# Optimization experiments

Measured on AMD Instinct MI355X. Metric: run time of the kernel, lower is better.

The kernel has to match this reference:

```python
import jax, jax.numpy as jnp
import numpy as np

N_NODES = 50000
N_EDGES = 800000
IN_FEATS = 128
SAGE_HID = 512
H_FEATS = 128
MLP_HID = 32
N_PARTS = 8


def setup_inputs() -> dict:
    key = jax.random.key(0)
    ks = jax.random.split(key, 16)
    s = 0.05
    return {
        "features": jax.random.normal(ks[0], (N_NODES, IN_FEATS), jnp.float32),
        "src": jax.random.randint(ks[1], (N_EDGES,), 0, N_NODES),
        "dst": jax.random.randint(ks[2], (N_EDGES,), 0, N_NODES),
        # SAGEConv layer 1 (in_feats -> 512): fc_self has bias, fc_neigh no bias
        "W1_self": jax.random.normal(ks[3], (IN_FEATS, SAGE_HID), jnp.float32) * s,
        "W1_neigh": jax.random.normal(ks[4], (IN_FEATS, SAGE_HID), jnp.float32) * s,
        "b1": jnp.zeros((SAGE_HID,), jnp.float32),
        # SAGEConv layer 2 (512 -> h_feats)
        "W2_self": jax.random.normal(ks[5], (SAGE_HID, H_FEATS), jnp.float32) * s,
        "W2_neigh": jax.random.normal(ks[6], (SAGE_HID, H_FEATS), jnp.float32) * s,
        "b2": jnp.zeros((H_FEATS,), jnp.float32),
        # Partitioning MLP
        "Wp1": jax.random.normal(ks[7], (H_FEATS, MLP_HID), jnp.float32) * s,
        "bp1": jnp.zeros((MLP_HID,), jnp.float32),
        "Wp2": jax.random.normal(ks[8], (MLP_HID, N_PARTS), jnp.float32) * s,
        "bp2": jnp.zeros((N_PARTS,), jnp.float32),
    }


def _sage_mean(x, src, dst, deg_inv, W_self, W_neigh, b):
    # gather source-node features per edge, sum by destination, divide by in-degree
    agg = jax.ops.segment_sum(jnp.take(x, src, axis=0), dst, num_segments=N_NODES)
    agg = agg * deg_inv[:, None]
    return x @ W_self + agg @ W_neigh + b


def reference(features, src, dst, W1_self, W1_neigh, b1, W2_self, W2_neigh, b2,
              Wp1, bp1, Wp2, bp2):
    deg = jax.ops.segment_sum(jnp.ones_like(dst, dtype=features.dtype), dst,
                              num_segments=N_NODES)
    deg_inv = 1.0 / jnp.maximum(deg, 1.0)
    h = jax.nn.relu(_sage_mean(features, src, dst, deg_inv, W1_self, W1_neigh, b1))
    h = jax.nn.relu(_sage_mean(h, src, dst, deg_inv, W2_self, W2_neigh, b2))
    x = jax.nn.relu(h @ Wp1 + bp1)
    logits = x @ Wp2 + bp2
    return jax.nn.softmax(logits, axis=1)
```

## Files before the change

### kernel.cpp

```cpp
#include <hip/hip_runtime.h>
#include <hip/hip_bf16.h>

#define N_NODES 50000
#define N_EDGES 800000

typedef short  short8  __attribute__((ext_vector_type(8)));
typedef float  floatx4 __attribute__((ext_vector_type(4)));

__device__ __forceinline__ short f2bf(float f) {
    union { __hip_bfloat16 h; short s; } u;
    u.h = __float2bfloat16(f);
    return u.s;
}
__device__ __forceinline__ float2 upk(unsigned v) {
    union { float f; unsigned u; } a, b;
    a.u = v << 16; b.u = v & 0xffff0000u;
    return make_float2(a.f, b.f);
}
__device__ __forceinline__ unsigned packbf(float lo, float hi) {
    return ((unsigned)(unsigned short)f2bf(hi) << 16) | (unsigned short)f2bf(lo);
}

__device__ __forceinline__ void gld_lds16(const short* g, short* l) {
    __builtin_amdgcn_global_load_lds(
        (const __attribute__((address_space(1))) int*)g,
        (__attribute__((address_space(3))) int*)l, 16, 0, 0);
}

__global__ void k_deg(const int* __restrict__ dst, int* __restrict__ deg) {
    int e = blockIdx.x * 256 + threadIdx.x;
    if (e < N_EDGES) atomicAdd(&deg[dst[e]], 1);
}

__global__ __launch_bounds__(1024) void k_scan1(const int* __restrict__ deg,
                                                int* __restrict__ bsum,
                                                float* __restrict__ dinv) {
    __shared__ int ws[16];
    int b = blockIdx.x, t = threadIdx.x, i = b * 1024 + t;
    int lane = t & 63, wid = t >> 6;
    int v = (i < N_NODES) ? deg[i] : 0;
    if (i < N_NODES) dinv[i] = 1.0f / fmaxf((float)v, 1.0f);
    int x = v;
    #pragma unroll
    for (int off = 1; off < 64; off <<= 1) x += __shfl_xor(x, off, 64);
    if (lane == 0) ws[wid] = x;
    __syncthreads();
    if (t == 0) {
        int s = 0;
        #pragma unroll
        for (int k = 0; k < 16; ++k) s += ws[k];
        bsum[b] = s;
    }
}

__global__ void k_scan2(const int* __restrict__ bsum, int* __restrict__ boff) {
    int lane = threadIdx.x;
    int v = (lane < 49) ? bsum[lane] : 0;
    int x = v;
    #pragma unroll
    for (int off = 1; off < 64; off <<= 1) {
        int y = __shfl_up(x, off, 64);
        if (lane >= off) x += y;
    }
    if (lane < 49) boff[lane] = x - v;
}

__global__ __launch_bounds__(1024) void k_scan3(const int* __restrict__ deg,
                                                const int* __restrict__ boff,
                                                int* __restrict__ rowptr,
                                                int* __restrict__ cursor) {
    __shared__ int ws[16];
    int b = blockIdx.x, t = threadIdx.x, i = b * 1024 + t;
    int lane = t & 63, wid = t >> 6;
    int v = (i < N_NODES) ? deg[i] : 0;
    int x = v;
    #pragma unroll
    for (int off = 1; off < 64; off <<= 1) {
        int y = __shfl_up(x, off, 64);
        if (lane >= off) x += y;
    }
    if (lane == 63) ws[wid] = x;
    __syncthreads();
    if (wid == 0) {
        int s = (lane < 16) ? ws[lane] : 0;
        #pragma unroll
        for (int off = 1; off < 16; off <<= 1) {
            int y = __shfl_up(s, off, 64);
            if (lane >= off) s += y;
        }
        if (lane < 16) ws[lane] = s;
    }
    __syncthreads();
    int waveOff = (wid == 0) ? 0 : ws[wid - 1];
    int incl = x + waveOff + boff[b];
    if (i < N_NODES) { rowptr[i + 1] = incl; cursor[i] = incl - v; }
    if (b == 0 && t == 0) rowptr[0] = 0;
}

__global__ void k_fill(const int* __restrict__ src, const int* __restrict__ dst,
                       int* __restrict__ cursor, int* __restrict__ col) {
    int e = blockIdx.x * 256 + threadIdx.x;
    if (e < N_EDGES) {
        int d = dst[e];
        int p = atomicAdd(&cursor[d], 1);
        col[p] = src[e];
    }
}

__global__ void k_cvt(const float* __restrict__ feat,
                      const float* __restrict__ W1s, const float* __restrict__ W1n,
                      const float* __restrict__ W2s, const float* __restrict__ W2n,
                      short* __restrict__ Abf, short* __restrict__ W1T,
                      short* __restrict__ W2T) {
    int bb = blockIdx.x, t = threadIdx.x;
    if (bb < 6250) {
        int idx = bb * 256 + t;
        if (idx >= N_NODES * 32) return;
        int n = idx >> 5, c = (idx & 31) * 4;
        float4 v = *(const float4*)(feat + (size_t)n * 128 + c);
        *(short4*)(Abf + (size_t)n * 256 + c) =
            make_short4(f2bf(v.x), f2bf(v.y), f2bf(v.z), f2bf(v.w));
    } else {
        int idx = (bb - 6250) * 256 + t;
        if (idx < 512 * 256) {
            int n = idx >> 8, k = idx & 255;
            float v = (k < 128) ? W1s[(size_t)k * 512 + n]
                                : W1n[(size_t)(k - 128) * 512 + n];
            W1T[idx] = f2bf(v);
        } else {
            int j = idx - 512 * 256;
            int n = j >> 9, k = j & 511;
            float v = (n < 128) ? W2s[(size_t)k * 128 + n]
                                : W2n[(size_t)k * 128 + (n - 128)];
            W2T[j] = f2bf(v);
        }
    }
}

template<int STRIDE>
__device__ __forceinline__ float2 wave_gather(
    const unsigned* __restrict__ U, const int* __restrict__ col,
    int s, int e, int lane) {
    float ax = 0.f, ay = 0.f;
    for (int base = s; base < e; base += 64) {
        int cnt = e - base; if (cnt > 64) cnt = 64;
        int myc = (base + lane < e) ? col[base + lane] : 0;
        int j = 0;
        for (; j + 16 <= cnt; j += 16) {
            unsigned v[16];
            #pragma unroll
            for (int u = 0; u < 16; ++u) {
                int c = __builtin_amdgcn_readlane(myc, j + u);
                v[u] = U[(size_t)c * STRIDE + lane];
            }
            #pragma unroll
            for (int u = 0; u < 16; ++u) {
                float2 f = upk(v[u]); ax += f.x; ay += f.y;
            }
        }
        for (; j + 8 <= cnt; j += 8) {
            unsigned v[8];
            #pragma unroll
            for (int u = 0; u < 8; ++u) {
                int c = __builtin_amdgcn_readlane(myc, j + u);
                v[u] = U[(size_t)c * STRIDE + lane];
            }
            #pragma unroll
            for (int u = 0; u < 8; ++u) {
                float2 f = upk(v[u]); ax += f.x; ay += f.y;
            }
        }
        if (j < cnt) {
            unsigned v[8];
            int m = cnt - j;
            #pragma unroll
            for (int u = 0; u < 8; ++u) {
                if (u < m) {
                    int c = __builtin_amdgcn_readlane(myc, j + u);
                    v[u] = U[(size_t)c * STRIDE + lane];
                }
            }
            #pragma unroll
            for (int u = 0; u < 8; ++u) {
                if (u < m) { float2 f = upk(v[u]); ax += f.x; ay += f.y; }
            }
        }
    }
    return make_float2(ax, ay);
}

__global__ __launch_bounds__(256) void k_agg(
    const unsigned* __restrict__ Au, const int* __restrict__ rowptr,
    const int* __restrict__ col, const float* __restrict__ dinv,
    unsigned* __restrict__ Aw) {
    int t = threadIdx.x, lane = t & 63, w = t >> 6;
    int n = blockIdx.x * 4 + w;
    int s = rowptr[n], e = rowptr[n + 1];
    float2 a = wave_gather<128>(Au, col, s, e, lane);
    float dv = dinv[n];
    Aw[(size_t)n * 128 + 64 + lane] = packbf(a.x * dv, a.y * dv);
}

__global__ __launch_bounds__(256) void k_aggmlp(
    const unsigned* __restrict__ Yu, const int* __restrict__ rowptr,
    const int* __restrict__ col, const float* __restrict__ dinv,
    const unsigned* __restrict__ Zu, const float* __restrict__ b2,
    const float* __restrict__ Wp1, const float* __restrict__ bp1,
    const float* __restrict__ Wp2, const float* __restrict__ bp2,
    float* __restrict__ out) {
    __shared__ float h2sh[4][128];
    __shared__ float xsh[4][32];
    int t = threadIdx.x, lane = t & 63, w = t >> 6;
    int n = blockIdx.x * 4 + w;
    int s = rowptr[n], e = rowptr[n + 1];
    float2 a = wave_gather<64>(Yu, col, s, e, lane);
    float dv = dinv[n];
    float2 zv = upk(Zu[(size_t)n * 64 + lane]);
    float2 bb = *(const float2*)(b2 + 2 * lane);
    h2sh[w][2 * lane]     = fmaxf(zv.x + a.x * dv + bb.x, 0.f);
    h2sh[w][2 * lane + 1] = fmaxf(zv.y + a.y * dv + bb.y, 0.f);
    int j = lane & 31, half = lane >> 5;
    float p = 0.f;
    #pragma unroll
    for (int k2 = 0; k2 < 64; ++k2) {
        int k = half * 64 + k2;
        p += h2sh[w][k] * Wp1[k * 32 + j];
    }
    p += __shfl_xor(p, 32, 64);
    if (half == 0) xsh[w][j] = fmaxf(p + bp1[j], 0.f);
    if (lane < 8) {
        float lg = bp2[lane];
        #pragma unroll
        for (int jj = 0; jj < 32; ++jj)
            lg += xsh[w][jj] * Wp2[jj * 8 + lane];
        float mx = lg;
        mx = fmaxf(mx, __shfl_xor(mx, 1, 64));
        mx = fmaxf(mx, __shfl_xor(mx, 2, 64));
        mx = fmaxf(mx, __shfl_xor(mx, 4, 64));
        float ev = expf(lg - mx);
        float sm = ev;
        sm += __shfl_xor(sm, 1, 64);
        sm += __shfl_xor(sm, 2, 64);
        sm += __shfl_xor(sm, 4, 64);
        out[(size_t)n * 8 + lane] = ev / sm;
    }
}

template<int K, int N, bool EPI1>
__global__ __launch_bounds__(256) void k_gemm_mfma(
    const short* __restrict__ A, const short* __restrict__ BT,
    const float* __restrict__ bias, short* __restrict__ Obf,
    short* __restrict__ Obf2) {
    __shared__ short smem[2 * 128 * 32];
    short* sA = smem;
    short* sB = smem + 128 * 32;
    short* sOut = smem;
    const int t = threadIdx.x;
    const int lane = t & 63;
    const int w = t >> 6;
    const int mBase = blockIdx.x * 128;
    const int nBase = blockIdx.y * 128;
    const int mOff = (w & 1) * 64;
    const int nOff = (w >> 1) * 64;

    floatx4 zero4 = {0.f, 0.f, 0.f, 0.f};
    floatx4 acc[4][4];
    #pragma unroll
    for (int i = 0; i < 4; ++i)
        #pragma unroll
        for (int j = 0; j < 4; ++j) acc[i][j] = zero4;

    const int rL = lane >> 2;
    const int cg = (((lane & 3) ^ ((lane >> 3) & 3))) * 8;
    const int rA = w * 32 + rL;
    const long gA0 = (long)min(mBase + rA,      N_NODES - 1) * K + cg;
    const long gA1 = (long)min(mBase + rA + 16, N_NODES - 1) * K + cg;
    const long gB0 = (long)(nBase + rA)      * K + cg;
    const long gB1 = (long)(nBase + rA + 16) * K + cg;
    short* lA0 = sA + (w * 32) * 32;
    short* lA1 = sA + (w * 32 + 16) * 32;
    short* lB0 = sB + (w * 32) * 32;
    short* lB1 = sB + (w * 32 + 16) * 32;

    const int fr = lane & 15;
    const int csel = (((lane >> 4) ^ ((lane >> 1) & 3))) * 8;

    for (int kt = 0; kt < K / 32; ++kt) {
        const int k0 = kt * 32;
        __syncthreads();
        gld_lds16(A + gA0 + k0, lA0);
        gld_lds16(A + gA1 + k0, lA1);
        gld_lds16(BT + gB0 + k0, lB0);
        gld_lds16(BT + gB1 + k0, lB1);
        __syncthreads();
        short8 af[4], bf[4];
        #pragma unroll
        for (int i = 0; i < 4; ++i) {
            af[i] = *(const short8*)(sA + (mOff + i * 16 + fr) * 32 + csel);
            bf[i] = *(const short8*)(sB + (nOff + i * 16 + fr) * 32 + csel);
        }
        #pragma unroll
        for (int mi = 0; mi < 4; ++mi)
            #pragma unroll
            for (int ni = 0; ni < 4; ++ni)
                acc[mi][ni] = __builtin_amdgcn_mfma_f32_16x16x32_bf16(
                    af[mi], bf[ni], acc[mi][ni], 0, 0, 0);
    }

    const int cn = lane & 15;
    const int cm = (lane >> 4) * 4;

    float bv[4];
    #pragma unroll
    for (int ni = 0; ni < 4; ++ni)
        bv[ni] = EPI1 ? bias[nBase + nOff + ni * 16 + cn] : 0.f;
    const int myh = mOff >> 6;
    const int ldc = EPI1 ? N : 128;
    const int cbase = EPI1 ? nBase : 0;
    short* target = EPI1 ? Obf : ((nBase < 128) ? Obf2 : Obf);
    for (int h = 0; h < 2; ++h) {
        __syncthreads();
        if (myh == h) {
            #pragma unroll
            for (int mi = 0; mi < 4; ++mi)
                #pragma unroll
                for (int ni = 0; ni < 4; ++ni)
                    #pragma unroll
                    for (int r = 0; r < 4; ++r) {
                        int mrow = mi * 16 + cm + r;
                        int nloc = nOff + ni * 16 + cn;
                        float v = acc[mi][ni][r];
                        if (EPI1) v = fmaxf(v + bv[ni], 0.f);
                        sOut[mrow * 128 + nloc] = f2bf(v);
                    }
        }
        __syncthreads();
        int r0 = t >> 2, c0 = (t & 3) * 32;
        int m = mBase + h * 64 + r0;
        if (m < N_NODES) {
            const short* sp = sOut + r0 * 128 + c0;
            short* gp = target + (size_t)m * ldc + cbase + c0;
            #pragma unroll
            for (int q = 0; q < 4; ++q)
                *(short8*)(gp + q * 8) = *(const short8*)(sp + q * 8);
        }
    }
}

extern "C" void kernel_launch(void* const* d_in, const int* in_sizes, int n_in,
                              void* d_out, int out_size, void* d_ws, size_t ws_size,
                              hipStream_t stream) {
    const float* feat   = (const float*)d_in[0];
    const int*   src    = (const int*)d_in[1];
    const int*   dst    = (const int*)d_in[2];
    const float* W1s    = (const float*)d_in[3];
    const float* W1n    = (const float*)d_in[4];
    const float* b1     = (const float*)d_in[5];
    const float* W2s    = (const float*)d_in[6];
    const float* W2n    = (const float*)d_in[7];
    const float* b2     = (const float*)d_in[8];
    const float* Wp1    = (const float*)d_in[9];
    const float* bp1    = (const float*)d_in[10];
    const float* Wp2    = (const float*)d_in[11];
    const float* bp2    = (const float*)d_in[12];
    float* out = (float*)d_out;

    char* w = (char*)d_ws;
    size_t off = 0;
    auto alloc = [&](size_t bytes) { char* p = w + off; off += (bytes + 255) & ~(size_t)255; return p; };
    int*   deg    = (int*)alloc(N_NODES * 4);
    int*   rowptr = (int*)alloc((N_NODES + 1) * 4);
    int*   cursor = (int*)alloc(N_NODES * 4);
    int*   col    = (int*)alloc(N_EDGES * 4);
    float* dinv   = (float*)alloc(N_NODES * 4);
    int*   bsum   = (int*)alloc(64 * 4);
    int*   boff   = (int*)alloc(64 * 4);
    short* Abf    = (short*)alloc((size_t)N_NODES * 256 * 2);
    short* W1T    = (short*)alloc((size_t)512 * 256 * 2);
    short* W2T    = (short*)alloc((size_t)256 * 512 * 2);
    short* h1bf   = (short*)alloc((size_t)N_NODES * 512 * 2);
    short* zbf    = (short*)alloc((size_t)N_NODES * 128 * 2);
    short* y1bf   = (short*)alloc((size_t)N_NODES * 128 * 2);

    hipMemsetAsync(deg, 0, N_NODES * 4, stream);
    k_deg<<<N_EDGES / 256, 256, 0, stream>>>(dst, deg);
    k_scan1<<<49, 1024, 0, stream>>>(deg, bsum, dinv);
    k_scan2<<<1, 64, 0, stream>>>(bsum, boff);
    k_scan3<<<49, 1024, 0, stream>>>(deg, boff, rowptr, cursor);
    k_fill<<<N_EDGES / 256, 256, 0, stream>>>(src, dst, cursor, col);
    k_cvt<<<7274, 256, 0, stream>>>(feat, W1s, W1n, W2s, W2n, Abf, W1T, W2T);
    k_agg<<<N_NODES / 4, 256, 0, stream>>>((const unsigned*)Abf, rowptr, col, dinv, (unsigned*)Abf);
    dim3 g1((N_NODES + 127) / 128, 4);
    k_gemm_mfma<256, 512, true><<<g1, 256, 0, stream>>>(Abf, W1T, b1, h1bf, nullptr);
    dim3 g2((N_NODES + 127) / 128, 2);
    k_gemm_mfma<512, 256, false><<<g2, 256, 0, stream>>>(h1bf, W2T, nullptr, y1bf, zbf);
    k_aggmlp<<<N_NODES / 4, 256, 0, stream>>>((const unsigned*)y1bf, rowptr, col, dinv,
                                              (const unsigned*)zbf, b2,
                                              Wp1, bp1, Wp2, bp2, out);
}
```

Before: 345.7 us.

## Gather neighbor features in FP8 to halve aggregation traffic

Input features and the layer-2 neighbor projection are now also written as packed FP8 (4 per 32-bit word). The two gather-aggregation kernels read these FP8 rows with each half-wave handling a different edge, then combine the halves with a cross-half shuffle. This halves the bytes moved by the random-access gathers, which dominate memory traffic. The cost is reduced numeric precision in the aggregated features, which risks exceeding the accuracy tolerance, plus an extra FP8 write pass in the conversion kernel.

Result: slower. 406.2 us (+17.5%).

```diff
diff --git a/kernel.cpp b/kernel.cpp
--- a/kernel.cpp
+++ b/kernel.cpp
@@ -6,6 +6,7 @@
 
 typedef short  short8  __attribute__((ext_vector_type(8)));
 typedef float  floatx4 __attribute__((ext_vector_type(4)));
+typedef float  floatx2 __attribute__((ext_vector_type(2)));
 
 __device__ __forceinline__ short f2bf(float f) {
     union { __hip_bfloat16 h; short s; } u;
@@ -19,6 +20,14 @@
 }
 __device__ __forceinline__ unsigned packbf(float lo, float hi) {
     return ((unsigned)(unsigned short)f2bf(hi) << 16) | (unsigned short)f2bf(lo);
+}
+__device__ __forceinline__ unsigned pack4fp8(float a, float b, float c, float d) {
+    int p = __builtin_amdgcn_cvt_pk_fp8_f32(a, b, 0, false);
+    p = __builtin_amdgcn_cvt_pk_fp8_f32(c, d, p, true);
+    return (unsigned)p;
+}
+__device__ __forceinline__ unsigned char fp8b(float v) {
+    return (unsigned char)(__builtin_amdgcn_cvt_pk_fp8_f32(v, v, 0, false) & 0xff);
 }
 
 __device__ __forceinline__ void gld_lds16(const short* g, short* l) {
@@ -110,8 +119,8 @@
 __global__ void k_cvt(const float* __restrict__ feat,
                       const float* __restrict__ W1s, const float* __restrict__ W1n,
                       const float* __restrict__ W2s, const float* __restrict__ W2n,
-                      short* __restrict__ Abf, short* __restrict__ W1T,
-                      short* __restrict__ W2T) {
+                      short* __restrict__ Abf, unsigned* __restrict__ F8u,
+                      short* __restrict__ W1T, short* __restrict__ W2T) {
     int bb = blockIdx.x, t = threadIdx.x;
     if (bb < 6250) {
         int idx = bb * 256 + t;
@@ -120,6 +129,7 @@
         float4 v = *(const float4*)(feat + (size_t)n * 128 + c);
         *(short4*)(Abf + (size_t)n * 256 + c) =
             make_short4(f2bf(v.x), f2bf(v.y), f2bf(v.z), f2bf(v.w));
+        F8u[(size_t)n * 32 + (c >> 2)] = pack4fp8(v.x, v.y, v.z, v.w);
     } else {
         int idx = (bb - 6250) * 256 + t;
         if (idx < 512 * 256) {
@@ -138,71 +148,104 @@
 }
 
 template<int STRIDE>
-__device__ __forceinline__ float2 wave_gather(
+__device__ __forceinline__ void wave_gather_fp8(
     const unsigned* __restrict__ U, const int* __restrict__ col,
-    int s, int e, int lane) {
-    float ax = 0.f, ay = 0.f;
+    int s, int e, int lane, float a[4]) {
+    const bool lo = lane < 32;
+    const int li = lane & 31;
+    a[0] = a[1] = a[2] = a[3] = 0.f;
     for (int base = s; base < e; base += 64) {
         int cnt = e - base; if (cnt > 64) cnt = 64;
         int myc = (base + lane < e) ? col[base + lane] : 0;
+        int pairs = cnt >> 1;
         int j = 0;
-        for (; j + 16 <= cnt; j += 16) {
+        for (; j + 16 <= pairs; j += 16) {
             unsigned v[16];
             #pragma unroll
             for (int u = 0; u < 16; ++u) {
-                int c = __builtin_amdgcn_readlane(myc, j + u);
-                v[u] = U[(size_t)c * STRIDE + lane];
+                int c0 = __builtin_amdgcn_readlane(myc, 2 * (j + u));
+                int c1 = __builtin_amdgcn_readlane(myc, 2 * (j + u) + 1);
+                int c = lo ? c0 : c1;
+                v[u] = U[(size_t)c * STRIDE + li];
             }
             #pragma unroll
             for (int u = 0; u < 16; ++u) {
-                float2 f = upk(v[u]); ax += f.x; ay += f.y;
-            }
-        }
-        for (; j + 8 <= cnt; j += 8) {
+                floatx2 f01 = __builtin_amdgcn_cvt_pk_f32_fp8(v[u], false);
+                floatx2 f23 = __builtin_amdgcn_cvt_pk_f32_fp8(v[u], true);
+                a[0] += f01.x; a[1] += f01.y; a[2] += f23.x; a[3] += f23.y;
+            }
+        }
+        for (; j + 8 <= pairs; j += 8) {
             unsigned v[8];
             #pragma unroll
             for (int u = 0; u < 8; ++u) {
-                int c = __builtin_amdgcn_readlane(myc, j + u);
-                v[u] = U[(size_t)c * STRIDE + lane];
+                int c0 = __builtin_amdgcn_readlane(myc, 2 * (j + u));
+                int c1 = __builtin_amdgcn_readlane(myc, 2 * (j + u) + 1);
+                int c = lo ? c0 : c1;
+                v[u] = U[(size_t)c * STRIDE + li];
             }
             #pragma unroll
             for (int u = 0; u < 8; ++u) {
-                float2 f = upk(v[u]); ax += f.x; ay += f.y;
-            }
-        }
-        if (j < cnt) {
+                floatx2 f01 = __builtin_amdgcn_cvt_pk_f32_fp8(v[u], false);
+                floatx2 f23 = __builtin_amdgcn_cvt_pk_f32_fp8(v[u], true);
+                a[0] += f01.x; a[1] += f01.y; a[2] += f23.x; a[3] += f23.y;
+            }
+        }
+        if (j < pairs) {
             unsigned v[8];
-            int m = cnt - j;
+            int m = pairs - j;
             #pragma unroll
             for (int u = 0; u < 8; ++u) {
                 if (u < m) {
-                    int c = __builtin_amdgcn_readlane(myc, j + u);
-                    v[u] = U[(size_t)c * STRIDE + lane];
+                    int c0 = __builtin_amdgcn_readlane(myc, 2 * (j + u));
+                    int c1 = __builtin_amdgcn_readlane(myc, 2 * (j + u) + 1);
+                    int c = lo ? c0 : c1;
+                    v[u] = U[(size_t)c * STRIDE + li];
                 }
             }
             #pragma unroll
             for (int u = 0; u < 8; ++u) {
-                if (u < m) { float2 f = upk(v[u]); ax += f.x; ay += f.y; }
-            }
-        }
-    }
-    return make_float2(ax, ay);
+                if (u < m) {
+                    floatx2 f01 = __builtin_amdgcn_cvt_pk_f32_fp8(v[u], false);
+                    floatx2 f23 = __builtin_amdgcn_cvt_pk_f32_fp8(v[u], true);
+                    a[0] += f01.x; a[1] += f01.y; a[2] += f23.x; a[3] += f23.y;
+                }
+            }
+        }
+        if (cnt & 1) {
+            int c = __builtin_amdgcn_readlane(myc, cnt - 1);
+            unsigned vv = U[(size_t)c * STRIDE + li];
+            if (lo) {
+                floatx2 f01 = __builtin_amdgcn_cvt_pk_f32_fp8(vv, false);
+                floatx2 f23 = __builtin_amdgcn_cvt_pk_f32_fp8(vv, true);
+                a[0] += f01.x; a[1] += f01.y; a[2] += f23.x; a[3] += f23.y;
+            }
+        }
+    }
+    #pragma unroll
+    for (int k = 0; k < 4; ++k) a[k] += __shfl_xor(a[k], 32, 64);
 }
 
 __global__ __launch_bounds__(256) void k_agg(
-    const unsigned* __restrict__ Au, const int* __restrict__ rowptr,
+    const unsigned* __restrict__ F8u, const int* __restrict__ rowptr,
     const int* __restrict__ col, const float* __restrict__ dinv,
     unsigned* __restrict__ Aw) {
     int t = threadIdx.x, lane = t & 63, w = t >> 6;
     int n = blockIdx.x * 4 + w;
     int s = rowptr[n], e = rowptr[n + 1];
-    float2 a = wave_gather<128>(Au, col, s, e, lane);
-    float dv = dinv[n];
-    Aw[(size_t)n * 128 + 64 + lane] = packbf(a.x * dv, a.y * dv);
+    float a[4];
+    wave_gather_fp8<32>(F8u, col, s, e, lane, a);
+    if (lane < 32) {
+        float dv = dinv[n];
+        uint2 o;
+        o.x = packbf(a[0] * dv, a[1] * dv);
+        o.y = packbf(a[2] * dv, a[3] * dv);
+        *(uint2*)(Aw + (size_t)n * 128 + 64 + lane * 2) = o;
+    }
 }
 
 __global__ __launch_bounds__(256) void k_aggmlp(
-    const unsigned* __restrict__ Yu, const int* __restrict__ rowptr,
+    const unsigned* __restrict__ Y8u, const int* __restrict__ rowptr,
     const int* __restrict__ col, const float* __restrict__ dinv,
     const unsigned* __restrict__ Zu, const float* __restrict__ b2,
     const float* __restrict__ Wp1, const float* __restrict__ bp1,
@@ -213,12 +256,18 @@
     int t = threadIdx.x, lane = t & 63, w = t >> 6;
     int n = blockIdx.x * 4 + w;
     int s = rowptr[n], e = rowptr[n + 1];
-    float2 a = wave_gather<64>(Yu, col, s, e, lane);
-    float dv = dinv[n];
-    float2 zv = upk(Zu[(size_t)n * 64 + lane]);
-    float2 bb = *(const float2*)(b2 + 2 * lane);
-    h2sh[w][2 * lane]     = fmaxf(zv.x + a.x * dv + bb.x, 0.f);
-    h2sh[w][2 * lane + 1] = fmaxf(zv.y + a.y * dv + bb.y, 0.f);
+    float a[4];
+    wave_gather_fp8<32>(Y8u, col, s, e, lane, a);
+    if (lane < 32) {
+        float dv = dinv[n];
+        uint2 zz = *(const uint2*)(Zu + (size_t)n * 64 + lane * 2);
+        float2 z01 = upk(zz.x), z23 = upk(zz.y);
+        float4 bb = *(const float4*)(b2 + lane * 4);
+        h2sh[w][lane * 4 + 0] = fmaxf(z01.x + a[0] * dv + bb.x, 0.f);
+        h2sh[w][lane * 4 + 1] = fmaxf(z01.y + a[1] * dv + bb.y, 0.f);
+        h2sh[w][lane * 4 + 2] = fmaxf(z23.x + a[2] * dv + bb.z, 0.f);
+        h2sh[w][lane * 4 + 3] = fmaxf(z23.y + a[3] * dv + bb.w, 0.f);
+    }
     int j = lane & 31, half = lane >> 5;
     float p = 0.f;
     #pragma unroll
@@ -250,11 +299,12 @@
 __global__ __launch_bounds__(256) void k_gemm_mfma(
     const short* __restrict__ A, const short* __restrict__ BT,
     const float* __restrict__ bias, short* __restrict__ Obf,
-    short* __restrict__ Obf2) {
+    short* __restrict__ Obf2, unsigned char* __restrict__ Y8) {
     __shared__ short smem[2 * 128 * 32];
     short* sA = smem;
     short* sB = smem + 128 * 32;
     short* sOut = smem;
+    unsigned char* sOutB = (unsigned char*)smem;
     const int t = threadIdx.x;
     const int lane = t & 63;
     const int w = t >> 6;
@@ -309,15 +359,16 @@
 
     const int cn = lane & 15;
     const int cm = (lane >> 4) * 4;
+    const int myh = mOff >> 6;
+    const bool toFp8 = (!EPI1) && (nBase >= 128);
 
     float bv[4];
     #pragma unroll
     for (int ni = 0; ni < 4; ++ni)
         bv[ni] = EPI1 ? bias[nBase + nOff + ni * 16 + cn] : 0.f;
-    const int myh = mOff >> 6;
     const int ldc = EPI1 ? N : 128;
     const int cbase = EPI1 ? nBase : 0;
-    short* target = EPI1 ? Obf : ((nBase < 128) ? Obf2 : Obf);
+    short* target = EPI1 ? Obf : Obf2;
     for (int h = 0; h < 2; ++h) {
         __syncthreads();
         if (myh == h) {
@@ -331,18 +382,30 @@
                         int nloc = nOff + ni * 16 + cn;
                         float v = acc[mi][ni][r];
                         if (EPI1) v = fmaxf(v + bv[ni], 0.f);
-                        sOut[mrow * 128 + nloc] = f2bf(v);
+                        if (toFp8) sOutB[mrow * 128 + nloc] = fp8b(v);
+                        else       sOut[mrow * 128 + nloc] = f2bf(v);
                     }
         }
         __syncthreads();
-        int r0 = t >> 2, c0 = (t & 3) * 32;
-        int m = mBase + h * 64 + r0;
-        if (m < N_NODES) {
-            const short* sp = sOut + r0 * 128 + c0;
-            short* gp = target + (size_t)m * ldc + cbase + c0;
-            #pragma unroll
-            for (int q = 0; q < 4; ++q)
-                *(short8*)(gp + q * 8) = *(const short8*)(sp + q * 8);
+        if (toFp8) {
+            int r0 = t >> 2, c0 = (t & 3) * 32;
+            int m = mBase + h * 64 + r0;
+            if (m < N_NODES) {
+                const unsigned char* sp = sOutB + r0 * 128 + c0;
+                unsigned char* gp = Y8 + (size_t)m * 128 + c0;
+                *(short8*)(gp) = *(const short8*)(sp);
+                *(short8*)(gp + 16) = *(const short8*)(sp + 16);
+            }
+        } else {
+            int r0 = t >> 2, c0 = (t & 3) * 32;
+            int m = mBase + h * 64 + r0;
+            if (m < N_NODES) {
+                const short* sp = sOut + r0 * 128 + c0;
+                short* gp = target + (size_t)m * ldc + cbase + c0;
+                #pragma unroll
+                for (int q = 0; q < 4; ++q)
+                    *(short8*)(gp + q * 8) = *(const short8*)(sp + q * 8);
+            }
         }
     }
 }
@@ -376,11 +439,12 @@
     int*   bsum   = (int*)alloc(64 * 4);
     int*   boff   = (int*)alloc(64 * 4);
     short* Abf    = (short*)alloc((size_t)N_NODES * 256 * 2);
+    unsigned* F8u = (unsigned*)alloc((size_t)N_NODES * 128);
     short* W1T    = (short*)alloc((size_t)512 * 256 * 2);
     short* W2T    = (short*)alloc((size_t)256 * 512 * 2);
     short* h1bf   = (short*)alloc((size_t)N_NODES * 512 * 2);
     short* zbf    = (short*)alloc((size_t)N_NODES * 128 * 2);
-    short* y1bf   = (short*)alloc((size_t)N_NODES * 128 * 2);
+    unsigned char* y8 = (unsigned char*)alloc((size_t)N_NODES * 128);
 
     hipMemsetAsync(deg, 0, N_NODES * 4, stream);
     k_deg<<<N_EDGES / 256, 256, 0, stream>>>(dst, deg);
@@ -388,13 +452,13 @@
     k_scan2<<<1, 64, 0, stream>>>(bsum, boff);
     k_scan3<<<49, 1024, 0, stream>>>(deg, boff, rowptr, cursor);
     k_fill<<<N_EDGES / 256, 256, 0, stream>>>(src, dst, cursor, col);
-    k_cvt<<<7274, 256, 0, stream>>>(feat, W1s, W1n, W2s, W2n, Abf, W1T, W2T);
-    k_agg<<<N_NODES / 4, 256, 0, stream>>>((const unsigned*)Abf, rowptr, col, dinv, (unsigned*)Abf);
+    k_cvt<<<7274, 256, 0, stream>>>(feat, W1s, W1n, W2s, W2n, Abf, F8u, W1T, W2T);
+    k_agg<<<N_NODES / 4, 256, 0, stream>>>(F8u, rowptr, col, dinv, (unsigned*)Abf);
     dim3 g1((N_NODES + 127) / 128, 4);
-    k_gemm_mfma<256, 512, true><<<g1, 256, 0, stream>>>(Abf, W1T, b1, h1bf, nullptr);
+    k_gemm_mfma<256, 512, true><<<g1, 256, 0, stream>>>(Abf, W1T, b1, h1bf, nullptr, nullptr);
     dim3 g2((N_NODES + 127) / 128, 2);
-    k_gemm_mfma<512, 256, false><<<g2, 256, 0, stream>>>(h1bf, W2T, nullptr, y1bf, zbf);
-    k_aggmlp<<<N_NODES / 4, 256, 0, stream>>>((const unsigned*)y1bf, rowptr, col, dinv,
+    k_gemm_mfma<512, 256, false><<<g2, 256, 0, stream>>>(h1bf, W2T, nullptr, nullptr, zbf, y8);
+    k_aggmlp<<<N_NODES / 4, 256, 0, stream>>>((const unsigned*)y8, rowptr, col, dinv,
                                               (const unsigned*)zbf, b2,
                                               Wp1, bp1, Wp2, bp2, out);
 }
```

## Store gathered neighbor features in FP8 to halve gather traffic

Applied to the files above, without the earlier changes.

Adds FP8 (e4m3/fnuz) copies of the input features and of the second-layer neighbor projection. The two edge-gather kernels now read 2 bytes per lane instead of 4 and convert with the hardware packed FP8-to-F32 instruction. This cuts memory traffic in the random-access aggregation, which dominates runtime. In exchange it loses accuracy in the neighbor sums and adds an extra FP8 write in the convert kernel and in the GEMM epilogue.

Result: no change. 342.3 us (-1.0%).

```diff
diff --git a/kernel.cpp b/kernel.cpp
--- a/kernel.cpp
+++ b/kernel.cpp
@@ -6,6 +6,7 @@
 
 typedef short  short8  __attribute__((ext_vector_type(8)));
 typedef float  floatx4 __attribute__((ext_vector_type(4)));
+typedef float  floatx2 __attribute__((ext_vector_type(2)));
 
 __device__ __forceinline__ short f2bf(float f) {
     union { __hip_bfloat16 h; short s; } u;
@@ -19,6 +20,14 @@
 }
 __device__ __forceinline__ unsigned packbf(float lo, float hi) {
     return ((unsigned)(unsigned short)f2bf(hi) << 16) | (unsigned short)f2bf(lo);
+}
+__device__ __forceinline__ unsigned pack4fp8(float a, float b, float c, float d) {
+    int p = __builtin_amdgcn_cvt_pk_fp8_f32(a, b, 0, false);
+    p = __builtin_amdgcn_cvt_pk_fp8_f32(c, d, p, true);
+    return (unsigned)p;
+}
+__device__ __forceinline__ unsigned char fp8b(float v) {
+    return (unsigned char)(__builtin_amdgcn_cvt_pk_fp8_f32(v, v, 0, false) & 0xff);
 }
 
 __device__ __forceinline__ void gld_lds16(const short* g, short* l) {
@@ -110,8 +119,8 @@
 __global__ void k_cvt(const float* __restrict__ feat,
                       const float* __restrict__ W1s, const float* __restrict__ W1n,
                       const float* __restrict__ W2s, const float* __restrict__ W2n,
-                      short* __restrict__ Abf, short* __restrict__ W1T,
-                      short* __restrict__ W2T) {
+                      short* __restrict__ Abf, unsigned* __restrict__ F8u,
+                      short* __restrict__ W1T, short* __restrict__ W2T) {
     int bb = blockIdx.x, t = threadIdx.x;
     if (bb < 6250) {
         int idx = bb * 256 + t;
@@ -120,6 +129,7 @@
         float4 v = *(const float4*)(feat + (size_t)n * 128 + c);
         *(short4*)(Abf + (size_t)n * 256 + c) =
             make_short4(f2bf(v.x), f2bf(v.y), f2bf(v.z), f2bf(v.w));
+        F8u[(size_t)n * 32 + (c >> 2)] = pack4fp8(v.x, v.y, v.z, v.w);
     } else {
         int idx = (bb - 6250) * 256 + t;
         if (idx < 512 * 256) {
@@ -138,8 +148,8 @@
 }
 
 template<int STRIDE>
-__device__ __forceinline__ float2 wave_gather(
-    const unsigned* __restrict__ U, const int* __restrict__ col,
+__device__ __forceinline__ float2 wave_gather8(
+    const unsigned short* __restrict__ U, const int* __restrict__ col,
     int s, int e, int lane) {
     float ax = 0.f, ay = 0.f;
     for (int base = s; base < e; base += 64) {
@@ -147,7 +157,7 @@
         int myc = (base + lane < e) ? col[base + lane] : 0;
         int j = 0;
         for (; j + 16 <= cnt; j += 16) {
-            unsigned v[16];
+            unsigned short v[16];
             #pragma unroll
             for (int u = 0; u < 16; ++u) {
                 int c = __builtin_amdgcn_readlane(myc, j + u);
@@ -155,11 +165,12 @@
             }
             #pragma unroll
             for (int u = 0; u < 16; ++u) {
-                float2 f = upk(v[u]); ax += f.x; ay += f.y;
+                floatx2 f = __builtin_amdgcn_cvt_pk_f32_fp8((unsigned)v[u], false);
+                ax += f.x; ay += f.y;
             }
         }
         for (; j + 8 <= cnt; j += 8) {
-            unsigned v[8];
+            unsigned short v[8];
             #pragma unroll
             for (int u = 0; u < 8; ++u) {
                 int c = __builtin_amdgcn_readlane(myc, j + u);
@@ -167,11 +178,12 @@
             }
             #pragma unroll
             for (int u = 0; u < 8; ++u) {
-                float2 f = upk(v[u]); ax += f.x; ay += f.y;
+                floatx2 f = __builtin_amdgcn_cvt_pk_f32_fp8((unsigned)v[u], false);
+                ax += f.x; ay += f.y;
             }
         }
         if (j < cnt) {
-            unsigned v[8];
+            unsigned short v[8];
             int m = cnt - j;
             #pragma unroll
             for (int u = 0; u < 8; ++u) {
@@ -182,7 +194,10 @@
             }
             #pragma unroll
             for (int u = 0; u < 8; ++u) {
-                if (u < m) { float2 f = upk(v[u]); ax += f.x; ay += f.y; }
+                if (u < m) {
+                    floatx2 f = __builtin_amdgcn_cvt_pk_f32_fp8((unsigned)v[u], false);
+                    ax += f.x; ay += f.y;
+                }
             }
         }
     }
@@ -190,19 +205,19 @@
 }
 
 __global__ __launch_bounds__(256) void k_agg(
-    const unsigned* __restrict__ Au, const int* __restrict__ rowptr,
+    const unsigned short* __restrict__ F8, const int* __restrict__ rowptr,
     const int* __restrict__ col, const float* __restrict__ dinv,
     unsigned* __restrict__ Aw) {
     int t = threadIdx.x, lane = t & 63, w = t >> 6;
     int n = blockIdx.x * 4 + w;
     int s = rowptr[n], e = rowptr[n + 1];
-    float2 a = wave_gather<128>(Au, col, s, e, lane);
+    float2 a = wave_gather8<64>(F8, col, s, e, lane);
     float dv = dinv[n];
     Aw[(size_t)n * 128 + 64 + lane] = packbf(a.x * dv, a.y * dv);
 }
 
 __global__ __launch_bounds__(256) void k_aggmlp(
-    const unsigned* __restrict__ Yu, const int* __restrict__ rowptr,
+    const unsigned short* __restrict__ Y8, const int* __restrict__ rowptr,
     const int* __restrict__ col, const float* __restrict__ dinv,
     const unsigned* __restrict__ Zu, const float* __restrict__ b2,
     const float* __restrict__ Wp1, const float* __restrict__ bp1,
@@ -213,7 +228,7 @@
     int t = threadIdx.x, lane = t & 63, w = t >> 6;
     int n = blockIdx.x * 4 + w;
     int s = rowptr[n], e = rowptr[n + 1];
-    float2 a = wave_gather<64>(Yu, col, s, e, lane);
+    float2 a = wave_gather8<64>(Y8, col, s, e, lane);
     float dv = dinv[n];
     float2 zv = upk(Zu[(size_t)n * 64 + lane]);
     float2 bb = *(const float2*)(b2 + 2 * lane);
@@ -250,11 +265,12 @@
 __global__ __launch_bounds__(256) void k_gemm_mfma(
     const short* __restrict__ A, const short* __restrict__ BT,
     const float* __restrict__ bias, short* __restrict__ Obf,
-    short* __restrict__ Obf2) {
+    short* __restrict__ Obf2, unsigned char* __restrict__ Y8) {
     __shared__ short smem[2 * 128 * 32];
     short* sA = smem;
     short* sB = smem + 128 * 32;
     short* sOut = smem;
+    unsigned char* sOutB = (unsigned char*)smem;
     const int t = threadIdx.x;
     const int lane = t & 63;
     const int w = t >> 6;
@@ -309,15 +325,16 @@
 
     const int cn = lane & 15;
     const int cm = (lane >> 4) * 4;
+    const int myh = mOff >> 6;
+    const bool toFp8 = (!EPI1) && (nBase >= 128);
 
     float bv[4];
     #pragma unroll
     for (int ni = 0; ni < 4; ++ni)
         bv[ni] = EPI1 ? bias[nBase + nOff + ni * 16 + cn] : 0.f;
-    const int myh = mOff >> 6;
     const int ldc = EPI1 ? N : 128;
     const int cbase = EPI1 ? nBase : 0;
-    short* target = EPI1 ? Obf : ((nBase < 128) ? Obf2 : Obf);
+    short* target = EPI1 ? Obf : Obf2;
     for (int h = 0; h < 2; ++h) {
         __syncthreads();
         if (myh == h) {
@@ -331,18 +348,30 @@
                         int nloc = nOff + ni * 16 + cn;
                         float v = acc[mi][ni][r];
                         if (EPI1) v = fmaxf(v + bv[ni], 0.f);
-                        sOut[mrow * 128 + nloc] = f2bf(v);
+                        if (toFp8) sOutB[mrow * 128 + nloc] = fp8b(v);
+                        else       sOut[mrow * 128 + nloc] = f2bf(v);
                     }
         }
         __syncthreads();
-        int r0 = t >> 2, c0 = (t & 3) * 32;
-        int m = mBase + h * 64 + r0;
-        if (m < N_NODES) {
-            const short* sp = sOut + r0 * 128 + c0;
-            short* gp = target + (size_t)m * ldc + cbase + c0;
-            #pragma unroll
-            for (int q = 0; q < 4; ++q)
-                *(short8*)(gp + q * 8) = *(const short8*)(sp + q * 8);
+        if (toFp8) {
+            int r0 = t >> 2, c0 = (t & 3) * 32;
+            int m = mBase + h * 64 + r0;
+            if (m < N_NODES) {
+                const unsigned char* sp = sOutB + r0 * 128 + c0;
+                unsigned char* gp = Y8 + (size_t)m * 128 + c0;
+                *(short8*)(gp) = *(const short8*)(sp);
+                *(short8*)(gp + 16) = *(const short8*)(sp + 16);
+            }
+        } else {
+            int r0 = t >> 2, c0 = (t & 3) * 32;
+            int m = mBase + h * 64 + r0;
+            if (m < N_NODES) {
+                const short* sp = sOut + r0 * 128 + c0;
+                short* gp = target + (size_t)m * ldc + cbase + c0;
+                #pragma unroll
+                for (int q = 0; q < 4; ++q)
+                    *(short8*)(gp + q * 8) = *(const short8*)(sp + q * 8);
+            }
         }
     }
 }
@@ -376,11 +405,12 @@
     int*   bsum   = (int*)alloc(64 * 4);
     int*   boff   = (int*)alloc(64 * 4);
     short* Abf    = (short*)alloc((size_t)N_NODES * 256 * 2);
+    unsigned* F8u = (unsigned*)alloc((size_t)N_NODES * 128);
     short* W1T    = (short*)alloc((size_t)512 * 256 * 2);
     short* W2T    = (short*)alloc((size_t)256 * 512 * 2);
     short* h1bf   = (short*)alloc((size_t)N_NODES * 512 * 2);
     short* zbf    = (short*)alloc((size_t)N_NODES * 128 * 2);
-    short* y1bf   = (short*)alloc((size_t)N_NODES * 128 * 2);
+    unsigned char* y8 = (unsigned char*)alloc((size_t)N_NODES * 128);
 
     hipMemsetAsync(deg, 0, N_NODES * 4, stream);
     k_deg<<<N_EDGES / 256, 256, 0, stream>>>(dst, deg);
@@ -388,13 +418,14 @@
     k_scan2<<<1, 64, 0, stream>>>(bsum, boff);
     k_scan3<<<49, 1024, 0, stream>>>(deg, boff, rowptr, cursor);
     k_fill<<<N_EDGES / 256, 256, 0, stream>>>(src, dst, cursor, col);
-    k_cvt<<<7274, 256, 0, stream>>>(feat, W1s, W1n, W2s, W2n, Abf, W1T, W2T);
-    k_agg<<<N_NODES / 4, 256, 0, stream>>>((const unsigned*)Abf, rowptr, col, dinv, (unsigned*)Abf);
+    k_cvt<<<7274, 256, 0, stream>>>(feat, W1s, W1n, W2s, W2n, Abf, F8u, W1T, W2T);
+    k_agg<<<N_NODES / 4, 256, 0, stream>>>((const unsigned short*)F8u, rowptr, col, dinv,
+                                           (unsigned*)Abf);
     dim3 g1((N_NODES + 127) / 128, 4);
-    k_gemm_mfma<256, 512, true><<<g1, 256, 0, stream>>>(Abf, W1T, b1, h1bf, nullptr);
+    k_gemm_mfma<256, 512, true><<<g1, 256, 0, stream>>>(Abf, W1T, b1, h1bf, nullptr, nullptr);
     dim3 g2((N_NODES + 127) / 128, 2);
-    k_gemm_mfma<512, 256, false><<<g2, 256, 0, stream>>>(h1bf, W2T, nullptr, y1bf, zbf);
-    k_aggmlp<<<N_NODES / 4, 256, 0, stream>>>((const unsigned*)y1bf, rowptr, col, dinv,
+    k_gemm_mfma<512, 256, false><<<g2, 256, 0, stream>>>(h1bf, W2T, nullptr, nullptr, zbf, y8);
+    k_aggmlp<<<N_NODES / 4, 256, 0, stream>>>((const unsigned short*)y8, rowptr, col, dinv,
                                               (const unsigned*)zbf, b2,
                                               Wp1, bp1, Wp2, bp2, out);
 }
```
